# Kernel optimization log

Measured on AMD Instinct MI355X. Metric: run time of the kernel, lower is better.

## Reference

```python
import jax, jax.numpy as jnp
import numpy as np

NUM_BINS = 8
TAIL = 3.0
MBW = 0.001  # min_bin_width
MBH = 0.001  # min_bin_height
MD = 0.001   # min_derivative


def _conv(x, w, b):
    y = jax.lax.conv_general_dilated(x, w, (1, 1), 'SAME',
                                     dimension_numbers=('NCHW', 'OIHW', 'NCHW'))
    return y + b[None, :, None, None]


def _convnet(x, w1, b1, w2, b2, w3, b3):
    h = jax.nn.relu(_conv(x, w1, b1))
    h = jax.nn.relu(_conv(h, w2, b2))
    return _conv(h, w3, b3)


def _rqs_forward(x, uw, uh, ud):
    # x: (N,), uw/uh: (N, num_bins), ud: (N, num_bins-1)
    nb = uw.shape[-1]
    inside = (x >= -TAIL) & (x <= TAIL)
    xin = jnp.clip(x, -TAIL, TAIL)
    # linear tails: pad derivatives so boundary slope == 1
    const = float(np.log(np.exp(1.0 - MD) - 1.0))
    ud = jnp.pad(ud, ((0, 0), (1, 1)), constant_values=const)

    widths = jax.nn.softmax(uw, axis=-1)
    widths = MBW + (1.0 - MBW * nb) * widths
    cumw = jnp.pad(jnp.cumsum(widths, axis=-1), ((0, 0), (1, 0)))
    cumw = 2.0 * TAIL * cumw - TAIL
    cumw = cumw.at[:, 0].set(-TAIL).at[:, -1].set(TAIL)
    widths = cumw[:, 1:] - cumw[:, :-1]

    heights = jax.nn.softmax(uh, axis=-1)
    heights = MBH + (1.0 - MBH * nb) * heights
    cumh = jnp.pad(jnp.cumsum(heights, axis=-1), ((0, 0), (1, 0)))
    cumh = 2.0 * TAIL * cumh - TAIL
    cumh = cumh.at[:, 0].set(-TAIL).at[:, -1].set(TAIL)
    heights = cumh[:, 1:] - cumh[:, :-1]

    deriv = MD + jax.nn.softplus(ud)  # (N, nb+1)

    # searchsorted: locate bin of each element
    idx = jnp.clip(jnp.sum((xin[:, None] >= cumw).astype(jnp.int32), axis=-1) - 1, 0, nb - 1)
    gather = lambda t: jnp.take_along_axis(t, idx[:, None], axis=-1)[:, 0]

    in_cw = gather(cumw)
    in_w = gather(widths)
    in_ch = gather(cumh)
    in_h = gather(heights)
    in_delta = gather(heights / widths)
    d0 = gather(deriv)
    d1 = gather(deriv[:, 1:])

    theta = (xin - in_cw) / in_w
    tom = theta * (1.0 - theta)
    numer = in_h * (in_delta * theta ** 2 + d0 * tom)
    denom = in_delta + (d0 + d1 - 2.0 * in_delta) * tom
    y = in_ch + numer / denom
    dnum = in_delta ** 2 * (d1 * theta ** 2 + 2.0 * in_delta * tom + d0 * (1.0 - theta) ** 2)
    lad = jnp.log(dnum) - 2.0 * jnp.log(denom)

    y = jnp.where(inside, y, x)
    lad = jnp.where(inside, lad, 0.0)
    return y, lad


def setup_inputs() -> dict:
    key = jax.random.key(0)
    ks = jax.random.split(key, 9)
    B, C, H, W = 32, 12, 64, 64
    hidden = 128
    cond_c = C // 3
    out_spline = C * (3 * NUM_BINS - 1)
    x = jax.random.normal(ks[0], (B, C, H, W), dtype=jnp.float32)
    logdet = jnp.zeros((B,), dtype=jnp.float32)
    conditioning = jax.random.normal(ks[1], (B, cond_c, H, W), dtype=jnp.float32)
    w1 = jax.random.normal(ks[2], (hidden, C + cond_c, 3, 3), dtype=jnp.float32) * 0.05
    b1 = jnp.zeros((hidden,), dtype=jnp.float32)
    w2 = jax.random.normal(ks[3], (hidden, hidden, 1, 1), dtype=jnp.float32) * 0.05
    b2 = jnp.zeros((hidden,), dtype=jnp.float32)
    w3 = jax.random.normal(ks[4], (out_spline, hidden, 3, 3), dtype=jnp.float32) * 0.01
    b3 = jnp.zeros((out_spline,), dtype=jnp.float32)
    return {"x": x, "logdet": logdet, "conditioning": conditioning,
            "w1": w1, "b1": b1, "w2": w2, "b2": b2, "w3": w3, "b3": b3}


def reference(x, logdet, conditioning, w1, b1, w2, b2, w3, b3):
    B, C, H, W = x.shape
    net_in = jnp.concatenate([x, conditioning], axis=1)
    params = _convnet(net_in, w1, b1, w2, b2, w3, b3)  # (B, C*(3nb-1), H, W)
    params = params.reshape(B, C, 3 * NUM_BINS - 1, H, W)
    params = params.transpose(0, 1, 3, 4, 2).reshape(B * C * H * W, 3 * NUM_BINS - 1)
    uw = params[:, :NUM_BINS]
    uh = params[:, NUM_BINS:2 * NUM_BINS]
    ud = params[:, 2 * NUM_BINS:]
    y_flat, lad_flat = _rqs_forward(x.reshape(-1), uw, uh, ud)
    y = y_flat.reshape(B, C, H, W)
    logdet_out = logdet + lad_flat.reshape(B, -1).sum(axis=1)
    return y, logdet_out
```

## Files before the change

### kernel.cpp

```cpp
#include <hip/hip_runtime.h>
#include <math.h>


#define NPIX 4096
#define NY   1572864

typedef _Float16 half8 __attribute__((ext_vector_type(8)));
typedef _Float16 half4 __attribute__((ext_vector_type(4)));
typedef float f32x4 __attribute__((ext_vector_type(4)));

#define ASYNC16(gsrc, ldst) \
  __builtin_amdgcn_global_load_lds((const __attribute__((address_space(1))) unsigned int*)(gsrc), \
                                   (__attribute__((address_space(3))) unsigned int*)(ldst), 16, 0, 0)

#define H2P_PLANE 4356
#define H2P_IDX(b, cc, pp) ((((size_t)(b) * 4 + (cc)) * H2P_PLANE + (pp)) << 5)
#define XH_IDX(b, pp) (((size_t)(b) * H2P_PLANE + (pp)) << 5)

__global__ __launch_bounds__(256) void prep_xh_k(
    const float* __restrict__ w1, const float* __restrict__ w2,
    const float* __restrict__ w3, _Float16* __restrict__ w1h,
    _Float16* __restrict__ w2h, _Float16* __restrict__ w3h,
    const float* __restrict__ logdet, float* __restrict__ ld_out,
    const float* __restrict__ x, const float* __restrict__ cond,
    _Float16* __restrict__ xh)
{
    const int i = blockIdx.x * 256 + threadIdx.x;
    if (i < 36864) {
        int k = i & 31, oc = (i >> 5) & 127, t = i >> 12;
        w1h[i] = (_Float16)((k < 16) ? w1[(oc * 16 + k) * 9 + t] : 0.f);
    }
    if (i < 16384) {
        int km = i & 31, oc = (i >> 5) & 127, ks = i >> 12;
        w2h[i] = (_Float16)w2[oc * 128 + ks * 32 + km];
    }
    {
        int cim = i & 31;
        int oc = (i >> 5) % 288;
        int tc = i / (288 * 32);
        int t = tc >> 2, cc = tc & 3;
        int c = oc / 24, j = oc % 24;
        int ci = cc * 32 + cim;
        float v = (j < 23) ? w3[((c * 23 + j) * 128 + ci) * 9 + t] : 0.f;
        w3h[i] = (_Float16)v;
    }
    if (i < 32) ld_out[i] = logdet[i];

    if (i < 139392) {
        const int b = i / H2P_PLANE, pp = i % H2P_PLANE;
        const int pr = pp / 66, pc = pp % 66;
        const bool interior = (pr >= 1) && (pr <= 64) && (pc >= 1) && (pc <= 64);
        _Float16 v[32];
#pragma unroll
        for (int ci = 0; ci < 32; ++ci) v[ci] = (_Float16)0.f;
        if (interior) {
            const int p = (pr - 1) * 64 + (pc - 1);
#pragma unroll
            for (int ci = 0; ci < 12; ++ci)
                v[ci] = (_Float16)x[((size_t)(b * 12 + ci) << 12) + p];
#pragma unroll
            for (int ci = 0; ci < 4; ++ci)
                v[12 + ci] = (_Float16)cond[((size_t)(b * 4 + ci) << 12) + p];
        }
        _Float16* dst = xh + ((size_t)i << 5);
#pragma unroll
        for (int q = 0; q < 4; ++q) *(f32x4*)(dst + q * 8) = *(f32x4*)(v + q * 8);
    }
}

__global__ __launch_bounds__(256, 2) void conv1_k(
    const _Float16* __restrict__ xh, const _Float16* __restrict__ w1h,
    const float* __restrict__ b1, _Float16* __restrict__ h1p)
{
    __shared__ __align__(16) char smem[73728];
    const int tid = threadIdx.x;
    const int wv = tid >> 6, lane = tid & 63;
    const int row16 = lane & 15, quad = lane >> 4;
    const int ptile = blockIdx.x;
    const int b = ptile >> 4;
    const int pim0 = (ptile & 15) << 8;
    const int h0 = pim0 >> 6;

#pragma unroll
    for (int k = 0; k < 18; ++k)
        ASYNC16(w1h + (size_t)(k * 256 + tid) * 8, smem + (k * 256 + wv * 64) * 16);

    f32x4 acc[4][8];
#pragma unroll
    for (int pt = 0; pt < 4; ++pt)
#pragma unroll
        for (int ot = 0; ot < 8; ++ot) acc[pt][ot] = (f32x4){0.f, 0.f, 0.f, 0.f};

    __syncthreads();
    const _Float16* wl = (const _Float16*)smem;

    for (int t = 0; t < 9; ++t) {
        const int dy = t / 3, dx = t % 3;
        const int pbase = (h0 + wv + dy) * 66 + dx + row16;
        half8 bf[4], af[8];
#pragma unroll
        for (int pt = 0; pt < 4; ++pt)
            bf[pt] = *(const half8*)(xh + XH_IDX(b, pbase + pt * 16) + quad * 8);
#pragma unroll
        for (int ot = 0; ot < 8; ++ot)
            af[ot] = *(const half8*)(wl + ((t * 128 + ot * 16 + row16) << 5) + quad * 8);
#pragma unroll
        for (int ot = 0; ot < 8; ++ot)
#pragma unroll
            for (int pt = 0; pt < 4; ++pt)
                acc[pt][ot] = __builtin_amdgcn_mfma_f32_16x16x32_f16(af[ot], bf[pt], acc[pt][ot], 0, 0, 0);
    }

    f32x4 bias[8];
#pragma unroll
    for (int ot = 0; ot < 8; ++ot) bias[ot] = *(const f32x4*)(b1 + ot * 16 + quad * 4);
#pragma unroll
    for (int pt = 0; pt < 4; ++pt) {
        const size_t pbase = ((size_t)((b << 12) + pim0 + wv * 64 + pt * 16 + row16)) << 7;
#pragma unroll
        for (int ot = 0; ot < 8; ++ot) {
            half4 v;
#pragma unroll
            for (int r = 0; r < 4; ++r)
                v[r] = (_Float16)fmaxf(acc[pt][ot][r] + bias[ot][r], 0.f);
            *(half4*)(h1p + pbase + ot * 16 + quad * 4) = v;
        }
    }
}

__global__ __launch_bounds__(256, 3) void conv2_k(
    const _Float16* __restrict__ h1p, const _Float16* __restrict__ w2h,
    const float* __restrict__ b2, _Float16* __restrict__ h2p)
{
    __shared__ __align__(16) char smem[33280];
    float* b2l = (float*)(smem + 32768);
    const int tid = threadIdx.x;
    const int wv = tid >> 6, lane = tid & 63;
    const int row16 = lane & 15, quad = lane >> 4;
    const int ptile = blockIdx.x;
    const int b = ptile >> 4;
    const int pim0 = (ptile & 15) << 8;

    if (tid < 128) b2l[tid] = b2[tid];
#pragma unroll
    for (int k = 0; k < 8; ++k) {
        const int c0 = k * 256 + wv * 64;
        ASYNC16(w2h + (size_t)(c0 + lane) * 8, smem + c0 * 16);
    }

    {
        const int base = blockIdx.x * 256 + tid;
#pragma unroll
        for (int rep = 0; rep < 2; ++rep) {
            const int i = base + rep * 131072;
            if (i < 133120) {
                const int q = i & 3;
                const int rest = i >> 2;
                const int r = rest % 260;
                const int cc2 = (rest / 260) & 3;
                const int bb = rest / 1040;
                int pp;
                if (r < 66)       pp = r;
                else if (r < 132) pp = 65 * 66 + (r - 66);
                else if (r < 196) pp = (r - 131) * 66;
                else              pp = (r - 195) * 66 + 65;
                f32x4 z = {0.f, 0.f, 0.f, 0.f};
                *(f32x4*)(h2p + H2P_IDX(bb, cc2, pp) + q * 8) = z;
            }
        }
    }

    f32x4 acc[4][8];
#pragma unroll
    for (int pt = 0; pt < 4; ++pt)
#pragma unroll
        for (int ot = 0; ot < 8; ++ot) acc[pt][ot] = (f32x4){0.f, 0.f, 0.f, 0.f};

    const int pixbase = (b << 12) + pim0 + wv * 64;
    __syncthreads();

#pragma unroll
    for (int ks = 0; ks < 4; ++ks) {
        half8 bf[4], af[8];
#pragma unroll
        for (int pt = 0; pt < 4; ++pt)
            bf[pt] = *(const half8*)(h1p + ((size_t)(pixbase + pt * 16 + row16) << 7) + ks * 32 + quad * 8);
        const _Float16* wl = (const _Float16*)smem;
#pragma unroll
        for (int ot = 0; ot < 8; ++ot)
            af[ot] = *(const half8*)(wl + ((ks * 128 + ot * 16 + row16) << 5) + quad * 8);
#pragma unroll
        for (int ot = 0; ot < 8; ++ot)
#pragma unroll
            for (int pt = 0; pt < 4; ++pt)
                acc[pt][ot] = __builtin_amdgcn_mfma_f32_16x16x32_f16(af[ot], bf[pt], acc[pt][ot], 0, 0, 0);
    }

#pragma unroll
    for (int pt = 0; pt < 4; ++pt) {
        const int p = pim0 + wv * 64 + pt * 16 + row16;
        const int pp = ((p >> 6) + 1) * 66 + (p & 63) + 1;
#pragma unroll
        for (int ot = 0; ot < 8; ++ot) {
            const int oc0 = ot * 16 + quad * 4;
            half4 v;
#pragma unroll
            for (int r = 0; r < 4; ++r)
                v[r] = (_Float16)fmaxf(acc[pt][ot][r] + b2l[oc0 + r], 0.f);
            *(half4*)(h2p + H2P_IDX(b, oc0 >> 5, pp) + (oc0 & 31)) = v;
        }
    }
}

__device__ __forceinline__ void rqs_eval(const f32x4* pv, float xv,
                                         float& yv_out, float& lad_out)
{
#define PRM(j) (pv[(j) >> 2][(j) & 3])
    const float xin = fminf(fmaxf(xv, -3.f), 3.f);

    float mw = PRM(0), mh = PRM(8);
#pragma unroll
    for (int j = 1; j < 8; ++j) { mw = fmaxf(mw, PRM(j)); mh = fmaxf(mh, PRM(8 + j)); }
    float ew[8], eh[8];
    float sw = 0.f, sh = 0.f;
#pragma unroll
    for (int j = 0; j < 8; ++j) {
        ew[j] = __expf(PRM(j) - mw);      sw += ew[j];
        eh[j] = __expf(PRM(8 + j) - mh);  sh += eh[j];
    }
    const float rw = 1.f / sw, rh = 1.f / sh;

    const float CONST_D = 0.5397423f;

    float cumw = 0.f, cumh = 0.f;
    float cw_lo = -3.f, ch_lo = -3.f;
    float in_cw = 0.f, in_w = 1.f, in_ch = 0.f, in_h = 1.f, sd0 = 0.f, sd1 = 0.f;
#pragma unroll
    for (int i = 0; i < 8; ++i) {
        cumw += fmaf(0.992f, ew[i] * rw, 0.001f);
        cumh += fmaf(0.992f, eh[i] * rh, 0.001f);
        const float cw_hi = (i == 7) ? 3.f : fmaf(6.f, cumw, -3.f);
        const float ch_hi = (i == 7) ? 3.f : fmaf(6.f, cumh, -3.f);
        const bool sel = (xin >= cw_lo) && ((i == 7) || (xin < cw_hi));
        in_cw = sel ? cw_lo : in_cw;
        in_w  = sel ? (cw_hi - cw_lo) : in_w;
        in_ch = sel ? ch_lo : in_ch;
        in_h  = sel ? (ch_hi - ch_lo) : in_h;
        sd0   = sel ? ((i == 0) ? CONST_D : PRM(16 + i - 1)) : sd0;
        sd1   = sel ? ((i == 7) ? CONST_D : PRM(16 + i)) : sd1;
        cw_lo = cw_hi; ch_lo = ch_hi;
    }

    const float d0 = 0.001f + ((sd0 > 20.f) ? sd0 : __logf(1.f + __expf(sd0)));
    const float d1 = 0.001f + ((sd1 > 20.f) ? sd1 : __logf(1.f + __expf(sd1)));

    const float r_inw = 1.f / in_w;
    const float delta = in_h * r_inw;
    const float theta = (xin - in_cw) * r_inw;
    const float omt = 1.f - theta;
    const float tom = theta * omt;
    const float th2 = theta * theta;
    const float numer = in_h * (delta * th2 + d0 * tom);
    const float denom = delta + (d0 + d1 - 2.f * delta) * tom;
    const float rden = 1.f / denom;
    float yv = in_ch + numer * rden;
    const float dnum = delta * delta * (d1 * th2 + 2.f * delta * tom + d0 * omt * omt);
    float lad = __logf(dnum * rden * rden);

    const bool inside = (xv >= -3.f) && (xv <= 3.f);
    yv_out = inside ? yv : xv;
    lad_out = inside ? lad : 0.f;
#undef PRM
}

__global__ __launch_bounds__(256, 3) void conv3_rqs_k(
    const _Float16* __restrict__ h2p, const _Float16* __restrict__ w3h,
    const float* __restrict__ b3, const float* __restrict__ x,
    float* __restrict__ y, float* __restrict__ ld_out)
{
    __shared__ __align__(16) char smem[38016];
    float* b3l = (float*)(smem + 37632);

    const int tid = threadIdx.x;
    const int wv = tid >> 6, lane = tid & 63;
    const int row16 = lane & 15, quad = lane >> 4;
    const int bid = blockIdx.x;
    const int g = bid / 24, r = bid % 24;
    const int col = r >> 3;
    const int ptile = (g << 3) | (r & 7);
    const int b = ptile >> 4;
    const int pim0 = (ptile & 15) << 8;
    const int h0 = pim0 >> 6;

    if (tid < 96) {
        const int c = tid / 24, j = tid % 24;
        b3l[tid] = (j < 23) ? b3[(col * 4 + c) * 23 + j] : 0.f;
    }

    f32x4 acc[4][6];
#pragma unroll
    for (int pt = 0; pt < 4; ++pt)
#pragma unroll
        for (int ot = 0; ot < 6; ++ot) acc[pt][ot] = (f32x4){0.f, 0.f, 0.f, 0.f};

    auto stage_wt = [&](int t, int cc, int buf) {
        const _Float16* gp = w3h + ((size_t)((t * 4 + cc) * 288 + col * 96) << 5);
        char* wb = smem + 25344 + buf * 6144;
        ASYNC16(gp + (size_t)tid * 8, wb + wv * 64 * 16);
        if (wv < 2) ASYNC16(gp + (size_t)(256 + tid) * 8, wb + (256 + wv * 64) * 16);
    };
    auto stage_act = [&](int cc) {
        const _Float16* ga = h2p + H2P_IDX(b, cc, h0 * 66);
#pragma unroll
        for (int k = 0; k < 6; ++k)
            ASYNC16(ga + (size_t)(k * 256 + tid) * 8, smem + (k * 256 + wv * 64) * 16);
        if (wv == 0 && lane < 48)
            ASYNC16(ga + (size_t)(1536 + lane) * 8, smem + 1536 * 16);
    };

    stage_act(0);
    stage_wt(0, 0, 0);

    for (int cc = 0; cc < 4; ++cc) {
        for (int t = 0; t < 9; ++t) {
            const int step = cc * 9 + t;
            __syncthreads();
            if (step + 1 < 36)
                stage_wt((t == 8) ? 0 : t + 1, (t == 8) ? cc + 1 : cc, (step + 1) & 1);
            const _Float16* act = (const _Float16*)smem;
            const _Float16* wt = (const _Float16*)(smem + 25344 + (step & 1) * 6144);
            const int dy = t / 3, dx = t % 3;
            const int lpp = (wv + dy) * 66 + dx + row16;
            half8 bf[4], af[6];
#pragma unroll
            for (int pt = 0; pt < 4; ++pt)
                bf[pt] = *(const half8*)(act + ((lpp + pt * 16) << 5) + quad * 8);
#pragma unroll
            for (int ot = 0; ot < 6; ++ot)
                af[ot] = *(const half8*)(wt + ((ot * 16 + row16) << 5) + quad * 8);
#pragma unroll
            for (int ot = 0; ot < 6; ++ot)
#pragma unroll
                for (int pt = 0; pt < 4; ++pt)
                    acc[pt][ot] = __builtin_amdgcn_mfma_f32_16x16x32_f16(af[ot], bf[pt], acc[pt][ot], 0, 0, 0);
            if (t == 8 && cc < 3) {
                __syncthreads();
                stage_act(cc + 1);
            }
        }
    }
    __syncthreads();

    float* epi = (float*)smem + wv * 1600;
    float lad_acc = 0.f;
#pragma unroll
    for (int pt = 0; pt < 4; ++pt) {
#pragma unroll
        for (int ot = 0; ot < 6; ++ot)
            *(f32x4*)(epi + row16 * 100 + ot * 16 + quad * 4) = acc[pt][ot];
        asm volatile("s_waitcnt lgkmcnt(0)" ::: "memory");
        __builtin_amdgcn_sched_barrier(0);
        {
            const int p16 = lane & 15, c = lane >> 4;
            const float* pb = epi + p16 * 100 + c * 24;
            const float* bb = b3l + c * 24;
            f32x4 pv[6];
#pragma unroll
            for (int q = 0; q < 6; ++q)
                pv[q] = *(const f32x4*)(pb + q * 4) + *(const f32x4*)(bb + q * 4);
            const int tpix = wv * 64 + pt * 16 + p16;
            const size_t xi = (((size_t)(b * 12 + col * 4 + c)) << 12) + (pim0 + tpix);
            const float xv = x[xi];
            float yv, lad;
            rqs_eval(pv, xv, yv, lad);
            y[xi] = yv;
            lad_acc += lad;
        }
        asm volatile("s_waitcnt lgkmcnt(0)" ::: "memory");
        __builtin_amdgcn_sched_barrier(0);
    }

#pragma unroll
    for (int off = 32; off > 0; off >>= 1) lad_acc += __shfl_down(lad_acc, off);
    if (lane == 0) atomicAdd(&ld_out[b], lad_acc);
}

extern "C" void kernel_launch(void* const* d_in, const int* in_sizes, int n_in,
                              void* d_out, int out_size, void* d_ws, size_t ws_size,
                              hipStream_t stream)
{
    const float* x      = (const float*)d_in[0];
    const float* logdet = (const float*)d_in[1];
    const float* cond   = (const float*)d_in[2];
    const float* w1     = (const float*)d_in[3];
    const float* b1     = (const float*)d_in[4];
    const float* w2     = (const float*)d_in[5];
    const float* b2     = (const float*)d_in[6];
    const float* w3     = (const float*)d_in[7];
    const float* b3     = (const float*)d_in[8];

    char* ws = (char*)d_ws;
    _Float16* h1p = (_Float16*)ws;
    _Float16* h2p = (_Float16*)(ws + 33554432);
    _Float16* xh  = (_Float16*)(ws + 33554432);
    _Float16* w1h = (_Float16*)(ws + 69238784);
    _Float16* w2h = (_Float16*)(ws + 69312512);
    _Float16* w3h = (_Float16*)(ws + 69345280);

    float* y      = (float*)d_out;
    float* ld_out = y + NY;

    prep_xh_k<<<1296, 256, 0, stream>>>(w1, w2, w3, w1h, w2h, w3h, logdet, ld_out, x, cond, xh);
    conv1_k<<<512, 256, 0, stream>>>(xh, w1h, b1, h1p);
    conv2_k<<<512, 256, 0, stream>>>(h1p, w2h, b2, h2p);
    conv3_rqs_k<<<1536, 256, 0, stream>>>(h2p, w3h, b3, x, y, ld_out);
}
```

Measured before the change: 239.5 us.

## Stage three conv3 weight taps per barrier to cut synchronization count

The conv3 loop now stages a whole row of three 3x3 taps into a larger double-buffered LDS region per step. This gives 12 barrier-separated steps instead of 36, with the three dx taps unrolled inside each step. The aim is to cut __syncthreads overhead and give the MFMA stream longer runs between barriers. In exchange, shared memory per block grows from about 38KB to about 62KB and launch bounds drop from 3 to 2 blocks per CU, which lowers occupancy and latency hiding.

```diff
diff --git a/kernel.cpp b/kernel.cpp
--- a/kernel.cpp
+++ b/kernel.cpp
@@ -273,13 +273,13 @@
 #undef PRM
 }
 
-__global__ __launch_bounds__(256, 3) void conv3_rqs_k(
+__global__ __launch_bounds__(256, 2) void conv3_rqs_k(
     const _Float16* __restrict__ h2p, const _Float16* __restrict__ w3h,
     const float* __restrict__ b3, const float* __restrict__ x,
     float* __restrict__ y, float* __restrict__ ld_out)
 {
-    __shared__ __align__(16) char smem[38016];
-    float* b3l = (float*)(smem + 37632);
+    __shared__ __align__(16) char smem[62592];
+    float* b3l = (float*)(smem + 62208);
 
     const int tid = threadIdx.x;
     const int wv = tid >> 6, lane = tid & 63;
@@ -303,11 +303,15 @@
 #pragma unroll
         for (int ot = 0; ot < 6; ++ot) acc[pt][ot] = (f32x4){0.f, 0.f, 0.f, 0.f};
 
-    auto stage_wt = [&](int t, int cc, int buf) {
-        const _Float16* gp = w3h + ((size_t)((t * 4 + cc) * 288 + col * 96) << 5);
-        char* wb = smem + 25344 + buf * 6144;
-        ASYNC16(gp + (size_t)tid * 8, wb + wv * 64 * 16);
-        if (wv < 2) ASYNC16(gp + (size_t)(256 + tid) * 8, wb + (256 + wv * 64) * 16);
+    auto stage_wt3 = [&](int dy, int cc, int buf) {
+#pragma unroll
+        for (int j = 0; j < 3; ++j) {
+            const int t = dy * 3 + j;
+            const _Float16* gp = w3h + ((size_t)((t * 4 + cc) * 288 + col * 96) << 5);
+            char* wb = smem + 25344 + buf * 18432 + j * 6144;
+            ASYNC16(gp + (size_t)tid * 8, wb + wv * 1024);
+            if (wv < 2) ASYNC16(gp + (size_t)(256 + tid) * 8, wb + 4096 + wv * 1024);
+        }
     };
     auto stage_act = [&](int cc) {
         const _Float16* ga = h2p + H2P_IDX(b, cc, h0 * 66);
@@ -319,31 +323,33 @@
     };
 
     stage_act(0);
-    stage_wt(0, 0, 0);
+    stage_wt3(0, 0, 0);
 
     for (int cc = 0; cc < 4; ++cc) {
-        for (int t = 0; t < 9; ++t) {
-            const int step = cc * 9 + t;
+        for (int dy = 0; dy < 3; ++dy) {
+            const int step = cc * 3 + dy;
             __syncthreads();
-            if (step + 1 < 36)
-                stage_wt((t == 8) ? 0 : t + 1, (t == 8) ? cc + 1 : cc, (step + 1) & 1);
+            if (step + 1 < 12)
+                stage_wt3((dy == 2) ? 0 : dy + 1, (dy == 2) ? cc + 1 : cc, (step + 1) & 1);
             const _Float16* act = (const _Float16*)smem;
-            const _Float16* wt = (const _Float16*)(smem + 25344 + (step & 1) * 6144);
-            const int dy = t / 3, dx = t % 3;
-            const int lpp = (wv + dy) * 66 + dx + row16;
-            half8 bf[4], af[6];
-#pragma unroll
-            for (int pt = 0; pt < 4; ++pt)
-                bf[pt] = *(const half8*)(act + ((lpp + pt * 16) << 5) + quad * 8);
-#pragma unroll
-            for (int ot = 0; ot < 6; ++ot)
-                af[ot] = *(const half8*)(wt + ((ot * 16 + row16) << 5) + quad * 8);
-#pragma unroll
-            for (int ot = 0; ot < 6; ++ot)
+            const _Float16* wt = (const _Float16*)(smem + 25344 + (step & 1) * 18432);
+            const int lrow = (wv + dy) * 66 + row16;
+#pragma unroll
+            for (int dx = 0; dx < 3; ++dx) {
+                half8 bf[4], af[6];
 #pragma unroll
                 for (int pt = 0; pt < 4; ++pt)
-                    acc[pt][ot] = __builtin_amdgcn_mfma_f32_16x16x32_f16(af[ot], bf[pt], acc[pt][ot], 0, 0, 0);
-            if (t == 8 && cc < 3) {
+                    bf[pt] = *(const half8*)(act + ((lrow + dx + pt * 16) << 5) + quad * 8);
+#pragma unroll
+                for (int ot = 0; ot < 6; ++ot)
+                    af[ot] = *(const half8*)(wt + dx * 3072 + ((ot * 16 + row16) << 5) + quad * 8);
+#pragma unroll
+                for (int ot = 0; ot < 6; ++ot)
+#pragma unroll
+                    for (int pt = 0; pt < 4; ++pt)
+                        acc[pt][ot] = __builtin_amdgcn_mfma_f32_16x16x32_f16(af[ot], bf[pt], acc[pt][ot], 0, 0, 0);
+            }
+            if (dy == 2 && cc < 3) {
                 __syncthreads();
                 stage_act(cc + 1);
             }
```

Result: faster. 223.0 us (-6.9%).
